# Optimization experiments

Measured on AMD Instinct MI355X. Metric: run time of the kernel, lower is better.

Reference implementation:

```python
import jax, jax.numpy as jnp
import numpy as np

N_ATOMS, N_BONDS, MAX_NB = 100000, 200000, 6
HIDDEN, DEPTH = 256, 6
ATOM_FDIM, BOND_FDIM = 39, 11


def setup_inputs() -> dict:
    key = jax.random.key(0)
    ks = jax.random.split(key, 6)
    fatoms = jax.random.normal(ks[0], (N_ATOMS, ATOM_FDIM), dtype=jnp.float32)
    fbonds = jax.random.normal(ks[1], (N_BONDS, BOND_FDIM), dtype=jnp.float32)
    # indices into message rows [0, N_BONDS); row 0 is the zero-padding row
    aoutgraph = jax.random.randint(ks[2], (N_ATOMS, MAX_NB), 0, N_BONDS)
    # (x, y) atom-index pairs; entry 0 is padding (unused)
    all_bonds = jax.random.randint(ks[3], (N_BONDS, 2), 0, N_ATOMS)
    # learned params (Linear layers, bias=False): y = x @ W.T
    W_nin = jax.random.normal(ks[4], (HIDDEN, ATOM_FDIM), dtype=jnp.float32) * 0.1
    W_node = jax.random.normal(ks[5], (HIDDEN, HIDDEN + BOND_FDIM), dtype=jnp.float32) * 0.05
    return {"fatoms": fatoms, "fbonds": fbonds, "aoutgraph": aoutgraph,
            "all_bonds": all_bonds, "W_nin": W_nin, "W_node": W_node}


def reference(fatoms, fbonds, aoutgraph, all_bonds, W_nin, W_node):
    # h0 = relu(W_nin @ fatoms); original keeps H_n as [hidden, n_atoms],
    # we keep [n_atoms, hidden] and transpose only at the end (same math).
    h0 = jax.nn.relu(fatoms @ W_nin.T)              # [N, H]
    in_n = all_bonds[1:, 1]                          # target atom of bonds 1..B-1
    zero_row = jnp.zeros((1, HIDDEN), dtype=h0.dtype)
    Hn = h0
    for _ in range(DEPTH):
        # message b = H_n[:, y_b] for b>=1, zero row at b=0, concat bond feats
        atom_msg = jnp.concatenate([zero_row, Hn[in_n]], axis=0)   # [B, H]
        message = jnp.concatenate([atom_msg, fbonds], axis=1)      # [B, H+11]
        # gather neighbor bond messages per atom and sum-aggregate
        nei = message[aoutgraph].sum(axis=1)                       # [N, H+11]
        Hn = jax.nn.relu(h0 + nei @ W_node.T)                      # [N, H]
    return Hn.T                                                    # [H, N] as original
```

## Files before the change

### kernel.cpp

```cpp
#include <hip/hip_runtime.h>

#define N_ATOMS 100000
#define N_BONDS 200000
#define MAX_NB 6
#define HIDDEN 256
#define DEPTH 6
#define ATOM_FDIM 39
#define BOND_FDIM 11
#define WNODE_COLS (HIDDEN + BOND_FDIM)

typedef __attribute__((ext_vector_type(8))) short bf16x8;
typedef __attribute__((ext_vector_type(4))) float f32x4;

__device__ __forceinline__ unsigned short f2bf(float x) {
  unsigned u = __float_as_uint(x);
  unsigned r = (u + 0x7FFFu + ((u >> 16) & 1u)) >> 16;
  return (unsigned short)r;
}
__device__ __forceinline__ float bf2f(unsigned short h) {
  return __uint_as_float(((unsigned)h) << 16);
}
__device__ __forceinline__ void split3(float x, short* s1, short* s2, short* s3) {
  unsigned short h1 = f2bf(x);
  float r1 = x - bf2f(h1);
  unsigned short h2 = f2bf(r1);
  float r2 = r1 - bf2f(h2);
  *s1 = (short)h1;
  *s2 = (short)h2;
  *s3 = (short)f2bf(r2);
}

union U8 { short s[8]; bf16x8 v; };

__global__ __launch_bounds__(256) void split_w_kernel(
    const float* __restrict__ W, short* __restrict__ Bsp) {
  int g = blockIdx.x * 256 + threadIdx.x;
  int n = g >> 6;
  int k4 = (g & 63) * 4;
  const float* wp = &W[(size_t)n * WNODE_COLS + k4];
  int o = n * 256 + k4;
#pragma unroll
  for (int j = 0; j < 4; ++j) {
    short a, b, c;
    split3(wp[j], &a, &b, &c);
    Bsp[o + j] = a;
    Bsp[65536 + o + j] = b;
    Bsp[131072 + o + j] = c;
  }
}

__global__ __launch_bounds__(256) void init_kernel(
    const float* __restrict__ fatoms,
    const float* __restrict__ fbonds,
    const int* __restrict__ aoutgraph,
    const float* __restrict__ W_nin,
    const float* __restrict__ W_node,
    float* __restrict__ Hn,
    float* __restrict__ base) {
  __shared__ float Wn_lds[ATOM_FDIM * 256];
  __shared__ float Wf_lds[BOND_FDIM * 256];
  __shared__ float fa_lds[32 * 40];
  __shared__ float fs_lds[32 * 12];
  int tid = threadIdx.x;
  int a0 = blockIdx.x * 32;

  for (int k = 0; k < ATOM_FDIM; ++k)
    Wn_lds[k * 256 + tid] = W_nin[tid * ATOM_FDIM + k];
  for (int k = 0; k < BOND_FDIM; ++k)
    Wf_lds[k * 256 + tid] = W_node[tid * WNODE_COLS + HIDDEN + k];
  {
    int a_l = tid >> 3, j8 = tid & 7;
#pragma unroll
    for (int jj = 0; jj < 5; ++jj) {
      int k = j8 * 5 + jj;
      if (k < ATOM_FDIM)
        fa_lds[a_l * 40 + k] = fatoms[(size_t)(a0 + a_l) * ATOM_FDIM + k];
    }
  }
  for (int i = tid; i < 384; i += 256) {
    int a_l = i / 12, f = i - a_l * 12;
    if (f < BOND_FDIM) {
      float s = 0.f;
#pragma unroll
      for (int nb = 0; nb < MAX_NB; ++nb) {
        int b = aoutgraph[(size_t)(a0 + a_l) * MAX_NB + nb];
        s += fbonds[(size_t)b * BOND_FDIM + f];
      }
      fs_lds[a_l * 12 + f] = s;
    }
  }
  __syncthreads();

  int l = tid & 63, w = tid >> 6;
  f32x4 acc1[8] = {};
  f32x4 acc2[8] = {};
  for (int k = 0; k < ATOM_FDIM; ++k) {
    f32x4 wv = *(const f32x4*)&Wn_lds[k * 256 + l * 4];
#pragma unroll
    for (int ai = 0; ai < 8; ++ai) {
      float av = fa_lds[(w * 8 + ai) * 40 + k];
      acc1[ai] += wv * av;
    }
  }
  for (int k = 0; k < BOND_FDIM; ++k) {
    f32x4 wv = *(const f32x4*)&Wf_lds[k * 256 + l * 4];
#pragma unroll
    for (int ai = 0; ai < 8; ++ai) {
      float av = fs_lds[(w * 8 + ai) * 12 + k];
      acc2[ai] += wv * av;
    }
  }
#pragma unroll
  for (int ai = 0; ai < 8; ++ai) {
    int a_g = a0 + w * 8 + ai;
    size_t off = (size_t)a_g * HIDDEN + l * 4;
    f32x4 h0v, bs;
#pragma unroll
    for (int j = 0; j < 4; ++j) {
      float h0j = fmaxf(acc1[ai][j], 0.f);
      h0v[j] = h0j;
      bs[j] = h0j + acc2[ai][j];
    }
    *(f32x4*)&Hn[off] = h0v;
    *(f32x4*)&base[off] = bs;
  }
}

#define KCH 32
#define AST 40

__global__ __launch_bounds__(256) void fused_kernel(
    const float* __restrict__ Hn_in,
    const float* __restrict__ base,
    const short* __restrict__ Bsp,
    const int* __restrict__ aout,
    const int* __restrict__ bonds,
    float* __restrict__ Hn_out) {
  __shared__ short As[2][3][64 * AST];
  __shared__ int src_lds[384];
  int tid = threadIdx.x;
  int a0 = blockIdx.x * 64;

  for (int i = tid; i < 384; i += 256) {
    int a_l = i / 6, nb = i - a_l * 6;
    int a = a0 + a_l;
    int s = -1;
    if (a < N_ATOMS) {
      int b = aout[(size_t)a * MAX_NB + nb];
      if (b != 0) s = bonds[2 * b + 1];
    }
    src_lds[i] = s;
  }
  __syncthreads();

  int lane = tid & 63, w = tid >> 6;
  int lr = lane & 15, lk = lane >> 4;
  int r_a = tid >> 2, q_a = tid & 3;

  const float* gp[MAX_NB];
  float gw[MAX_NB];
#pragma unroll
  for (int nb = 0; nb < MAX_NB; ++nb) {
    int s = src_lds[r_a * 6 + nb];
    int sr = s >= 0 ? s : 0;
    gw[nb] = s >= 0 ? 1.f : 0.f;
    gp[nb] = &Hn_in[(size_t)sr * HIDDEN + q_a * 8];
  }
  int ao_st = r_a * AST + q_a * 8;

  f32x4 acc[4][4] = {};

  {
    f32x4 vlo = {0.f, 0.f, 0.f, 0.f}, vhi = {0.f, 0.f, 0.f, 0.f};
#pragma unroll
    for (int nb = 0; nb < MAX_NB; ++nb) {
      vlo += *(const f32x4*)(gp[nb]) * gw[nb];
      vhi += *(const f32x4*)(gp[nb] + 4) * gw[nb];
    }
    U8 t1, t2, t3;
#pragma unroll
    for (int j = 0; j < 4; ++j) split3(vlo[j], &t1.s[j], &t2.s[j], &t3.s[j]);
#pragma unroll
    for (int j = 0; j < 4; ++j)
      split3(vhi[j], &t1.s[4 + j], &t2.s[4 + j], &t3.s[4 + j]);
    *(bf16x8*)&As[0][0][ao_st] = t1.v;
    *(bf16x8*)&As[0][1][ao_st] = t2.v;
    *(bf16x8*)&As[0][2][ao_st] = t3.v;
  }
  __syncthreads();

#pragma unroll
  for (int c = 0; c < 8; ++c) {
    const int cur = c & 1;
    bf16x8 b0[4], b1[4], b2[4];
#pragma unroll
    for (int n = 0; n < 4; ++n) {
      int bo = (w * 64 + n * 16 + lr) * 256 + c * KCH + lk * 8;
      b0[n] = *(const bf16x8*)&Bsp[bo];
      b1[n] = *(const bf16x8*)&Bsp[65536 + bo];
      b2[n] = *(const bf16x8*)&Bsp[131072 + bo];
    }
    f32x4 ga[MAX_NB], gb[MAX_NB];
    if (c < 7) {
      const int k1 = (c + 1) * KCH;
#pragma unroll
      for (int nb = 0; nb < MAX_NB; ++nb) {
        ga[nb] = *(const f32x4*)(gp[nb] + k1);
        gb[nb] = *(const f32x4*)(gp[nb] + k1 + 4);
      }
    }
    __builtin_amdgcn_sched_barrier(0);
    __builtin_amdgcn_s_setprio(1);
#pragma unroll
    for (int m = 0; m < 4; ++m) {
      int ao = (m * 16 + lr) * AST + lk * 8;
      bf16x8 af0 = *(const bf16x8*)&As[cur][0][ao];
      bf16x8 af1 = *(const bf16x8*)&As[cur][1][ao];
      bf16x8 af2 = *(const bf16x8*)&As[cur][2][ao];
#pragma unroll
      for (int n = 0; n < 4; ++n) {
        f32x4 cc = acc[m][n];
        cc = __builtin_amdgcn_mfma_f32_16x16x32_bf16(af0, b0[n], cc, 0, 0, 0);
        cc = __builtin_amdgcn_mfma_f32_16x16x32_bf16(af0, b1[n], cc, 0, 0, 0);
        cc = __builtin_amdgcn_mfma_f32_16x16x32_bf16(af1, b0[n], cc, 0, 0, 0);
        cc = __builtin_amdgcn_mfma_f32_16x16x32_bf16(af1, b1[n], cc, 0, 0, 0);
        cc = __builtin_amdgcn_mfma_f32_16x16x32_bf16(af0, b2[n], cc, 0, 0, 0);
        cc = __builtin_amdgcn_mfma_f32_16x16x32_bf16(af2, b0[n], cc, 0, 0, 0);
        acc[m][n] = cc;
      }
    }
    __builtin_amdgcn_s_setprio(0);
    if (c < 7) {
      f32x4 vlo = {0.f, 0.f, 0.f, 0.f}, vhi = {0.f, 0.f, 0.f, 0.f};
#pragma unroll
      for (int nb = 0; nb < MAX_NB; ++nb) {
        vlo += ga[nb] * gw[nb];
        vhi += gb[nb] * gw[nb];
      }
      U8 t1, t2, t3;
#pragma unroll
      for (int j = 0; j < 4; ++j) split3(vlo[j], &t1.s[j], &t2.s[j], &t3.s[j]);
#pragma unroll
      for (int j = 0; j < 4; ++j)
        split3(vhi[j], &t1.s[4 + j], &t2.s[4 + j], &t3.s[4 + j]);
      *(bf16x8*)&As[cur ^ 1][0][ao_st] = t1.v;
      *(bf16x8*)&As[cur ^ 1][1][ao_st] = t2.v;
      *(bf16x8*)&As[cur ^ 1][2][ao_st] = t3.v;
      __syncthreads();
    }
  }

#pragma unroll
  for (int m = 0; m < 4; ++m) {
    int row0 = a0 + m * 16 + lk * 4;
#pragma unroll
    for (int n = 0; n < 4; ++n) {
      int col = w * 64 + n * 16 + lr;
#pragma unroll
      for (int r = 0; r < 4; ++r) {
        int row = row0 + r;
        if (row < N_ATOMS) {
          size_t off = (size_t)row * HIDDEN + col;
          float v = fmaxf(base[off] + acc[m][n][r], 0.f);
          __builtin_nontemporal_store(v, &Hn_out[off]);
        }
      }
    }
  }
}

__global__ __launch_bounds__(256) void transpose_kernel(
    const float* __restrict__ Hn, float* __restrict__ out) {
  __shared__ float tile[64][68];
  int a0 = blockIdx.x * 64, h0 = blockIdx.y * 64;
  int tid = threadIdx.x;
#pragma unroll
  for (int p = 0; p < 2; ++p) {
    int id = tid + p * 256;
    int r = id >> 3, c8 = (id & 7) * 8;
    int ag = a0 + r;
    if (ag > N_ATOMS - 1) ag = N_ATOMS - 1;
    const float* hp = &Hn[(size_t)ag * HIDDEN + h0 + c8];
    *(f32x4*)&tile[r][c8] = *(const f32x4*)hp;
    *(f32x4*)&tile[r][c8 + 4] = *(const f32x4*)(hp + 4);
  }
  __syncthreads();
  int h = tid >> 2, as = (tid & 3) * 16;
  size_t ob = (size_t)(h0 + h) * N_ATOMS + a0 + as;
  if (a0 + 64 <= N_ATOMS) {
#pragma unroll
    for (int q = 0; q < 4; ++q) {
      f32x4 v;
#pragma unroll
      for (int j = 0; j < 4; ++j) v[j] = tile[as + q * 4 + j][h];
      __builtin_nontemporal_store(v, (f32x4*)&out[ob + q * 4]);
    }
  } else {
    for (int j = 0; j < 16; ++j)
      if (a0 + as + j < N_ATOMS)
        __builtin_nontemporal_store(tile[as + j][h], &out[ob + j]);
  }
}

extern "C" void kernel_launch(void* const* d_in, const int* in_sizes, int n_in,
                              void* d_out, int out_size, void* d_ws, size_t ws_size,
                              hipStream_t stream) {
  const float* fatoms = (const float*)d_in[0];
  const float* fbonds = (const float*)d_in[1];
  const int* aoutgraph = (const int*)d_in[2];
  const int* all_bonds = (const int*)d_in[3];
  const float* W_nin = (const float*)d_in[4];
  const float* W_node = (const float*)d_in[5];
  float* out = (float*)d_out;

  const size_t NH = (size_t)N_ATOMS * HIDDEN;
  float* base = (float*)d_ws;
  float* HnA = base + NH;
  short* Bsp = (short*)(HnA + NH);
  float* HnB = out;

  split_w_kernel<<<64, 256, 0, stream>>>(W_node, Bsp);
  init_kernel<<<N_ATOMS / 32, 256, 0, stream>>>(fatoms, fbonds, aoutgraph,
                                                W_nin, W_node, HnA, base);

  const int nblk = (N_ATOMS + 63) / 64;
  for (int it = 0; it < DEPTH; ++it) {
    const float* in = (it & 1) ? HnB : HnA;
    float* o = (it & 1) ? HnA : HnB;
    fused_kernel<<<nblk, 256, 0, stream>>>(in, base, Bsp, aoutgraph,
                                           all_bonds, o);
  }
  dim3 tgrid(nblk, HIDDEN / 64);
  transpose_kernel<<<tgrid, 256, 0, stream>>>(HnA, out);
}
```

Before: 1.484 ms.

## Split fused gather+GEMM into separate gather and GEMM kernels per layer

Replaces the fused per-layer kernel, which gathered neighbor rows inside the GEMM's K loop, with a standalone gather kernel that writes the summed neighbor features to a scratch buffer (the output array), followed by a GEMM kernel that streams that buffer. The aim is to free the GEMM from latency-bound random gathers and register pressure, and to let it run at higher occupancy through launch bounds. The cost is an extra full N×H write and read per layer plus an extra launch.

```diff
diff --git a/kernel.cpp b/kernel.cpp
--- a/kernel.cpp
+++ b/kernel.cpp
@@ -126,57 +126,51 @@
   }
 }
 
+__global__ __launch_bounds__(256) void gather_kernel(
+    const float* __restrict__ Hn,
+    const int* __restrict__ aout,
+    const int* __restrict__ bonds,
+    float* __restrict__ Nsum) {
+  int a = blockIdx.x * 4 + (threadIdx.x >> 6);
+  int l = threadIdx.x & 63;
+  const int* ap = &aout[(size_t)a * MAX_NB];
+  f32x4 s = {0.f, 0.f, 0.f, 0.f};
+#pragma unroll
+  for (int nb = 0; nb < MAX_NB; ++nb) {
+    int b = ap[nb];
+    if (b != 0) {
+      int src = bonds[2 * b + 1];
+      s += *(const f32x4*)&Hn[(size_t)src * HIDDEN + l * 4];
+    }
+  }
+  __builtin_nontemporal_store(s, (f32x4*)&Nsum[(size_t)a * HIDDEN + l * 4]);
+}
+
 #define KCH 32
 #define AST 40
 
-__global__ __launch_bounds__(256) void fused_kernel(
-    const float* __restrict__ Hn_in,
+__global__ __launch_bounds__(256, 3) void gemm_kernel(
+    const float* __restrict__ Nsum,
     const float* __restrict__ base,
     const short* __restrict__ Bsp,
-    const int* __restrict__ aout,
-    const int* __restrict__ bonds,
+    const int* __restrict__ dummy,
     float* __restrict__ Hn_out) {
   __shared__ short As[2][3][64 * AST];
-  __shared__ int src_lds[384];
   int tid = threadIdx.x;
   int a0 = blockIdx.x * 64;
-
-  for (int i = tid; i < 384; i += 256) {
-    int a_l = i / 6, nb = i - a_l * 6;
-    int a = a0 + a_l;
-    int s = -1;
-    if (a < N_ATOMS) {
-      int b = aout[(size_t)a * MAX_NB + nb];
-      if (b != 0) s = bonds[2 * b + 1];
-    }
-    src_lds[i] = s;
-  }
-  __syncthreads();
-
   int lane = tid & 63, w = tid >> 6;
   int lr = lane & 15, lk = lane >> 4;
   int r_a = tid >> 2, q_a = tid & 3;
-
-  const float* gp[MAX_NB];
-  float gw[MAX_NB];
-#pragma unroll
-  for (int nb = 0; nb < MAX_NB; ++nb) {
-    int s = src_lds[r_a * 6 + nb];
-    int sr = s >= 0 ? s : 0;
-    gw[nb] = s >= 0 ? 1.f : 0.f;
-    gp[nb] = &Hn_in[(size_t)sr * HIDDEN + q_a * 8];
-  }
+  int rg = a0 + r_a;
+  if (rg > N_ATOMS - 1) rg = N_ATOMS - 1;
+  const float* np = &Nsum[(size_t)rg * HIDDEN + q_a * 8];
   int ao_st = r_a * AST + q_a * 8;
 
   f32x4 acc[4][4] = {};
 
   {
-    f32x4 vlo = {0.f, 0.f, 0.f, 0.f}, vhi = {0.f, 0.f, 0.f, 0.f};
-#pragma unroll
-    for (int nb = 0; nb < MAX_NB; ++nb) {
-      vlo += *(const f32x4*)(gp[nb]) * gw[nb];
-      vhi += *(const f32x4*)(gp[nb] + 4) * gw[nb];
-    }
+    f32x4 vlo = __builtin_nontemporal_load((const f32x4*)np);
+    f32x4 vhi = __builtin_nontemporal_load((const f32x4*)(np + 4));
     U8 t1, t2, t3;
 #pragma unroll
     for (int j = 0; j < 4; ++j) split3(vlo[j], &t1.s[j], &t2.s[j], &t3.s[j]);
@@ -200,14 +194,11 @@
       b1[n] = *(const bf16x8*)&Bsp[65536 + bo];
       b2[n] = *(const bf16x8*)&Bsp[131072 + bo];
     }
-    f32x4 ga[MAX_NB], gb[MAX_NB];
+    f32x4 va = {0.f, 0.f, 0.f, 0.f}, vb = {0.f, 0.f, 0.f, 0.f};
     if (c < 7) {
       const int k1 = (c + 1) * KCH;
-#pragma unroll
-      for (int nb = 0; nb < MAX_NB; ++nb) {
-        ga[nb] = *(const f32x4*)(gp[nb] + k1);
-        gb[nb] = *(const f32x4*)(gp[nb] + k1 + 4);
-      }
+      va = __builtin_nontemporal_load((const f32x4*)(np + k1));
+      vb = __builtin_nontemporal_load((const f32x4*)(np + k1 + 4));
     }
     __builtin_amdgcn_sched_barrier(0);
     __builtin_amdgcn_s_setprio(1);
@@ -231,18 +222,12 @@
     }
     __builtin_amdgcn_s_setprio(0);
     if (c < 7) {
-      f32x4 vlo = {0.f, 0.f, 0.f, 0.f}, vhi = {0.f, 0.f, 0.f, 0.f};
-#pragma unroll
-      for (int nb = 0; nb < MAX_NB; ++nb) {
-        vlo += ga[nb] * gw[nb];
-        vhi += gb[nb] * gw[nb];
-      }
       U8 t1, t2, t3;
 #pragma unroll
-      for (int j = 0; j < 4; ++j) split3(vlo[j], &t1.s[j], &t2.s[j], &t3.s[j]);
+      for (int j = 0; j < 4; ++j) split3(va[j], &t1.s[j], &t2.s[j], &t3.s[j]);
 #pragma unroll
       for (int j = 0; j < 4; ++j)
-        split3(vhi[j], &t1.s[4 + j], &t2.s[4 + j], &t3.s[4 + j]);
+        split3(vb[j], &t1.s[4 + j], &t2.s[4 + j], &t3.s[4 + j]);
       *(bf16x8*)&As[cur ^ 1][0][ao_st] = t1.v;
       *(bf16x8*)&As[cur ^ 1][1][ao_st] = t2.v;
       *(bf16x8*)&As[cur ^ 1][2][ao_st] = t3.v;
@@ -261,8 +246,7 @@
         int row = row0 + r;
         if (row < N_ATOMS) {
           size_t off = (size_t)row * HIDDEN + col;
-          float v = fmaxf(base[off] + acc[m][n][r], 0.f);
-          __builtin_nontemporal_store(v, &Hn_out[off]);
+          Hn_out[off] = fmaxf(base[off] + acc[m][n][r], 0.f);
         }
       }
     }
@@ -315,21 +299,20 @@
 
   const size_t NH = (size_t)N_ATOMS * HIDDEN;
   float* base = (float*)d_ws;
-  float* HnA = base + NH;
-  short* Bsp = (short*)(HnA + NH);
-  float* HnB = out;
+  float* Hn = base + NH;
+  short* Bsp = (short*)(Hn + NH);
+  float* Nsum = out;
 
   split_w_kernel<<<64, 256, 0, stream>>>(W_node, Bsp);
   init_kernel<<<N_ATOMS / 32, 256, 0, stream>>>(fatoms, fbonds, aoutgraph,
-                                                W_nin, W_node, HnA, base);
+                                                W_nin, W_node, Hn, base);
 
   const int nblk = (N_ATOMS + 63) / 64;
   for (int it = 0; it < DEPTH; ++it) {
-    const float* in = (it & 1) ? HnB : HnA;
-    float* o = (it & 1) ? HnA : HnB;
-    fused_kernel<<<nblk, 256, 0, stream>>>(in, base, Bsp, aoutgraph,
-                                           all_bonds, o);
+    gather_kernel<<<N_ATOMS / 4, 256, 0, stream>>>(Hn, aoutgraph, all_bonds,
+                                                   Nsum);
+    gemm_kernel<<<nblk, 256, 0, stream>>>(Nsum, base, Bsp, nullptr, Hn);
   }
   dim3 tgrid(nblk, HIDDEN / 64);
-  transpose_kernel<<<tgrid, 256, 0, stream>>>(HnA, out);
-}
+  transpose_kernel<<<tgrid, 256, 0, stream>>>(Hn, out);
+}
```

New measurement: 1.768 ms. +19.2%, slower.

## Halve fused kernel atom tile to 32 rows and raise occupancy

Applied to the files above, without the earlier changes.

The fused gather+GEMM kernel now processes 32 atoms per block instead of 64. Each thread gathers one float4 per neighbor instead of two, using 32-bit byte offsets rather than 64-bit pointers, and the kernel requests 3 blocks per CU through launch bounds. Bounds checks are dropped because N_ATOMS divides evenly by 32. The aim is more in-flight blocks and fewer registers to hide the random gather latency. In exchange each block re-reads the full split weight matrix for half as many rows, which doubles total B-operand traffic.

```diff
diff --git a/kernel.cpp b/kernel.cpp
--- a/kernel.cpp
+++ b/kernel.cpp
@@ -10,6 +10,7 @@
 #define WNODE_COLS (HIDDEN + BOND_FDIM)
 
 typedef __attribute__((ext_vector_type(8))) short bf16x8;
+typedef __attribute__((ext_vector_type(4))) short s16x4;
 typedef __attribute__((ext_vector_type(4))) float f32x4;
 
 __device__ __forceinline__ unsigned short f2bf(float x) {
@@ -30,7 +31,7 @@
   *s3 = (short)f2bf(r2);
 }
 
-union U8 { short s[8]; bf16x8 v; };
+union U4 { short s[4]; s16x4 v; };
 
 __global__ __launch_bounds__(256) void split_w_kernel(
     const float* __restrict__ W, short* __restrict__ Bsp) {
@@ -129,63 +130,54 @@
 #define KCH 32
 #define AST 40
 
-__global__ __launch_bounds__(256) void fused_kernel(
+__global__ __launch_bounds__(256, 3) void fused_kernel(
     const float* __restrict__ Hn_in,
     const float* __restrict__ base,
     const short* __restrict__ Bsp,
     const int* __restrict__ aout,
     const int* __restrict__ bonds,
     float* __restrict__ Hn_out) {
-  __shared__ short As[2][3][64 * AST];
-  __shared__ int src_lds[384];
+  __shared__ short As[2][3][32 * AST];
+  __shared__ int src_lds[192];
   int tid = threadIdx.x;
-  int a0 = blockIdx.x * 64;
-
-  for (int i = tid; i < 384; i += 256) {
-    int a_l = i / 6, nb = i - a_l * 6;
-    int a = a0 + a_l;
-    int s = -1;
-    if (a < N_ATOMS) {
-      int b = aout[(size_t)a * MAX_NB + nb];
-      if (b != 0) s = bonds[2 * b + 1];
-    }
-    src_lds[i] = s;
+  int a0 = blockIdx.x * 32;
+
+  if (tid < 192) {
+    int a_l = tid / 6, nb = tid - a_l * 6;
+    int b = aout[(size_t)(a0 + a_l) * MAX_NB + nb];
+    src_lds[tid] = (b != 0) ? bonds[2 * b + 1] : -1;
   }
   __syncthreads();
 
   int lane = tid & 63, w = tid >> 6;
   int lr = lane & 15, lk = lane >> 4;
-  int r_a = tid >> 2, q_a = tid & 3;
-
-  const float* gp[MAX_NB];
+  int r_a = tid >> 3, q = tid & 7;
+
+  const char* hb = (const char*)Hn_in;
+  unsigned voff[MAX_NB];
   float gw[MAX_NB];
 #pragma unroll
   for (int nb = 0; nb < MAX_NB; ++nb) {
     int s = src_lds[r_a * 6 + nb];
     int sr = s >= 0 ? s : 0;
     gw[nb] = s >= 0 ? 1.f : 0.f;
-    gp[nb] = &Hn_in[(size_t)sr * HIDDEN + q_a * 8];
-  }
-  int ao_st = r_a * AST + q_a * 8;
-
-  f32x4 acc[4][4] = {};
+    voff[nb] = (unsigned)((sr * HIDDEN + q * 4) * 4);
+  }
+  int ao_st = r_a * AST + q * 4;
+
+  f32x4 acc[2][4] = {};
 
   {
-    f32x4 vlo = {0.f, 0.f, 0.f, 0.f}, vhi = {0.f, 0.f, 0.f, 0.f};
-#pragma unroll
-    for (int nb = 0; nb < MAX_NB; ++nb) {
-      vlo += *(const f32x4*)(gp[nb]) * gw[nb];
-      vhi += *(const f32x4*)(gp[nb] + 4) * gw[nb];
-    }
-    U8 t1, t2, t3;
-#pragma unroll
-    for (int j = 0; j < 4; ++j) split3(vlo[j], &t1.s[j], &t2.s[j], &t3.s[j]);
-#pragma unroll
-    for (int j = 0; j < 4; ++j)
-      split3(vhi[j], &t1.s[4 + j], &t2.s[4 + j], &t3.s[4 + j]);
-    *(bf16x8*)&As[0][0][ao_st] = t1.v;
-    *(bf16x8*)&As[0][1][ao_st] = t2.v;
-    *(bf16x8*)&As[0][2][ao_st] = t3.v;
+    f32x4 v = {0.f, 0.f, 0.f, 0.f};
+#pragma unroll
+    for (int nb = 0; nb < MAX_NB; ++nb)
+      v += *(const f32x4*)(hb + voff[nb]) * gw[nb];
+    U4 t1, t2, t3;
+#pragma unroll
+    for (int j = 0; j < 4; ++j) split3(v[j], &t1.s[j], &t2.s[j], &t3.s[j]);
+    *(s16x4*)&As[0][0][ao_st] = t1.v;
+    *(s16x4*)&As[0][1][ao_st] = t2.v;
+    *(s16x4*)&As[0][2][ao_st] = t3.v;
   }
   __syncthreads();
 
@@ -200,19 +192,16 @@
       b1[n] = *(const bf16x8*)&Bsp[65536 + bo];
       b2[n] = *(const bf16x8*)&Bsp[131072 + bo];
     }
-    f32x4 ga[MAX_NB], gb[MAX_NB];
+    f32x4 ga[MAX_NB];
     if (c < 7) {
-      const int k1 = (c + 1) * KCH;
-#pragma unroll
-      for (int nb = 0; nb < MAX_NB; ++nb) {
-        ga[nb] = *(const f32x4*)(gp[nb] + k1);
-        gb[nb] = *(const f32x4*)(gp[nb] + k1 + 4);
-      }
+#pragma unroll
+      for (int nb = 0; nb < MAX_NB; ++nb)
+        ga[nb] = *(const f32x4*)(hb + voff[nb] + (c + 1) * KCH * 4);
     }
     __builtin_amdgcn_sched_barrier(0);
     __builtin_amdgcn_s_setprio(1);
 #pragma unroll
-    for (int m = 0; m < 4; ++m) {
+    for (int m = 0; m < 2; ++m) {
       int ao = (m * 16 + lr) * AST + lk * 8;
       bf16x8 af0 = *(const bf16x8*)&As[cur][0][ao];
       bf16x8 af1 = *(const bf16x8*)&As[cur][1][ao];
@@ -231,39 +220,30 @@
     }
     __builtin_amdgcn_s_setprio(0);
     if (c < 7) {
-      f32x4 vlo = {0.f, 0.f, 0.f, 0.f}, vhi = {0.f, 0.f, 0.f, 0.f};
-#pragma unroll
-      for (int nb = 0; nb < MAX_NB; ++nb) {
-        vlo += ga[nb] * gw[nb];
-        vhi += gb[nb] * gw[nb];
-      }
-      U8 t1, t2, t3;
-#pragma unroll
-      for (int j = 0; j < 4; ++j) split3(vlo[j], &t1.s[j], &t2.s[j], &t3.s[j]);
-#pragma unroll
-      for (int j = 0; j < 4; ++j)
-        split3(vhi[j], &t1.s[4 + j], &t2.s[4 + j], &t3.s[4 + j]);
-      *(bf16x8*)&As[cur ^ 1][0][ao_st] = t1.v;
-      *(bf16x8*)&As[cur ^ 1][1][ao_st] = t2.v;
-      *(bf16x8*)&As[cur ^ 1][2][ao_st] = t3.v;
+      f32x4 v = {0.f, 0.f, 0.f, 0.f};
+#pragma unroll
+      for (int nb = 0; nb < MAX_NB; ++nb) v += ga[nb] * gw[nb];
+      U4 t1, t2, t3;
+#pragma unroll
+      for (int j = 0; j < 4; ++j) split3(v[j], &t1.s[j], &t2.s[j], &t3.s[j]);
+      *(s16x4*)&As[cur ^ 1][0][ao_st] = t1.v;
+      *(s16x4*)&As[cur ^ 1][1][ao_st] = t2.v;
+      *(s16x4*)&As[cur ^ 1][2][ao_st] = t3.v;
       __syncthreads();
     }
   }
 
 #pragma unroll
-  for (int m = 0; m < 4; ++m) {
+  for (int m = 0; m < 2; ++m) {
     int row0 = a0 + m * 16 + lk * 4;
 #pragma unroll
     for (int n = 0; n < 4; ++n) {
       int col = w * 64 + n * 16 + lr;
 #pragma unroll
       for (int r = 0; r < 4; ++r) {
-        int row = row0 + r;
-        if (row < N_ATOMS) {
-          size_t off = (size_t)row * HIDDEN + col;
-          float v = fmaxf(base[off] + acc[m][n][r], 0.f);
-          __builtin_nontemporal_store(v, &Hn_out[off]);
-        }
+        size_t off = (size_t)(row0 + r) * HIDDEN + col;
+        float v = fmaxf(base[off] + acc[m][n][r], 0.f);
+        __builtin_nontemporal_store(v, &Hn_out[off]);
       }
     }
   }
@@ -323,13 +303,13 @@
   init_kernel<<<N_ATOMS / 32, 256, 0, stream>>>(fatoms, fbonds, aoutgraph,
                                                 W_nin, W_node, HnA, base);
 
-  const int nblk = (N_ATOMS + 63) / 64;
+  const int nblk = N_ATOMS / 32;
   for (int it = 0; it < DEPTH; ++it) {
     const float* in = (it & 1) ? HnB : HnA;
     float* o = (it & 1) ? HnA : HnB;
     fused_kernel<<<nblk, 256, 0, stream>>>(in, base, Bsp, aoutgraph,
                                            all_bonds, o);
   }
-  dim3 tgrid(nblk, HIDDEN / 64);
+  dim3 tgrid((N_ATOMS + 63) / 64, HIDDEN / 64);
   transpose_kernel<<<tgrid, 256, 0, stream>>>(HnA, out);
 }
```

Result: faster. 1.443 ms (-2.7%).
